# Kernel tuning notes

Hardware: AMD Instinct MI355X
Metric: run time of the kernel (lower is better)

The kernel has to match this reference:

```python
import jax, jax.numpy as jnp
import numpy as np

N_NODES = 100000
IN_F = 128
H_F = 128
LOOKBACK = 3
N_EDGES = 640000


def setup_inputs() -> dict:
    key = jax.random.key(0)
    ks = jax.random.split(key, 16)
    s = lambda k, shp: jax.random.normal(k, shp, dtype=jnp.float32) * 0.05
    inp = {
        "feat": jax.random.normal(ks[0], (N_NODES, IN_F), dtype=jnp.float32),
        "edges": jax.random.randint(ks[1], (LOOKBACK, 2, N_EDGES), 0, N_NODES, dtype=jnp.int32),
        # conv1 (SAGEConv pool, in->h) params
        "Wp1": s(ks[2], (IN_F, IN_F)), "bp1": jnp.zeros((IN_F,), jnp.float32),
        "Ws1": s(ks[3], (H_F, IN_F)), "Wn1": s(ks[4], (H_F, IN_F)), "b1": jnp.zeros((H_F,), jnp.float32),
        # BatchNorm1d affine params (training-mode batch stats)
        "gamma": jnp.ones((H_F,), jnp.float32), "beta": jnp.zeros((H_F,), jnp.float32),
        # conv2 (SAGEConv pool, h->h) params
        "Wp2": s(ks[5], (H_F, H_F)), "bp2": jnp.zeros((H_F,), jnp.float32),
        "Ws2": s(ks[6], (H_F, H_F)), "Wn2": s(ks[7], (H_F, H_F)), "b2": jnp.zeros((H_F,), jnp.float32),
    }
    return inp


def _sage_pool_conv(h, src, dst, Wp, bp, Ws, Wn, b):
    # pool aggregator: m = relu(fc_pool(h)); neigh = max over in-edges
    m = jax.nn.relu(h @ Wp.T + bp)                      # [N, d]
    agg = jax.ops.segment_max(m[src], dst, num_segments=N_NODES)  # [N, d]
    agg = jnp.where(jnp.isfinite(agg), agg, 0.0)        # nodes with no in-edges -> 0
    return h @ Ws.T + agg @ Wn.T + b


def _batchnorm(x, gamma, beta, eps=1e-5):
    mu = jnp.mean(x, axis=0)
    var = jnp.var(x, axis=0)
    return (x - mu) * jax.lax.rsqrt(var + eps) * gamma + beta


def reference(feat, edges, Wp1, bp1, Ws1, Wn1, b1, gamma, beta, Wp2, bp2, Ws2, Wn2, b2):
    def per_graph(e):
        src, dst = e[0], e[1]
        h = _sage_pool_conv(feat, src, dst, Wp1, bp1, Ws1, Wn1, b1)
        h = _batchnorm(h, gamma, beta)
        h = jax.nn.relu(h)
        h = _sage_pool_conv(h, src, dst, Wp2, bp2, Ws2, Wn2, b2)
        return h

    return jax.vmap(per_graph)(edges)  # [lookback, N, H_F]
```

## Files before the change

### kernel.cpp

```cpp
#include <hip/hip_runtime.h>
#include <hip/hip_bf16.h>

#define NNODES 100000
#define FD 128
#define NEDGES 640000
#define NB 391
#define GEMM_GRID 782
#define OFFS_U32 100032

typedef __bf16 bf16x8 __attribute__((ext_vector_type(8)));
typedef __bf16 bf16x4 __attribute__((ext_vector_type(4)));
typedef float f32x4 __attribute__((ext_vector_type(4)));
typedef unsigned short u16x8 __attribute__((ext_vector_type(8)));

__device__ __forceinline__ bf16x8 cvt8(float4 a, float4 b) {
  bf16x8 r;
  r[0] = (__bf16)a.x; r[1] = (__bf16)a.y; r[2] = (__bf16)a.z; r[3] = (__bf16)a.w;
  r[4] = (__bf16)b.x; r[5] = (__bf16)b.y; r[6] = (__bf16)b.z; r[7] = (__bf16)b.w;
  return r;
}

__global__ __launch_bounds__(256) void packw6_k(
    const float* __restrict__ W0, const float* __restrict__ W1,
    const float* __restrict__ W2, const float* __restrict__ W3,
    const float* __restrict__ W4, const float* __restrict__ W5,
    __bf16* __restrict__ out) {
  const int gidx = blockIdx.x * 256 + threadIdx.x;
  const int wi = gidx >> 11;
  const int f = gidx & 2047;
  const float* W = wi == 0 ? W0 : wi == 1 ? W1 : wi == 2 ? W2
                 : wi == 3 ? W3 : wi == 4 ? W4 : W5;
  const int c = f >> 8, kk = (f >> 6) & 3, lane = f & 63;
  const int lr = lane & 15, lg = lane >> 4;
  const float* p = W + (c * 16 + lr) * FD + kk * 32 + lg * 8;
  *(bf16x8*)(out + (long)gidx * 8) = cvt8(*(const float4*)p, *(const float4*)(p + 4));
}

template <int AM>
__device__ __forceinline__ void load_arow(const void* __restrict__ A, long row,
                                          int kbase, const float* __restrict__ scsh,
                                          bf16x8 (&af)[4]) {
  if constexpr (AM == 1) {
#pragma unroll
    for (int kk = 0; kk < 4; ++kk)
      af[kk] = *(const bf16x8*)((const __bf16*)A + row * FD + kbase + kk * 32);
  } else if constexpr (AM == 3) {
#pragma unroll
    for (int kk = 0; kk < 4; ++kk) {
      const int k = kbase + kk * 32;
      const bf16x8 r = *(const bf16x8*)((const __bf16*)A + row * FD + k);
      const float4 scx = *(const float4*)(scsh + k);
      const float4 scy = *(const float4*)(scsh + k + 4);
      const float4 shx = *(const float4*)(scsh + 128 + k);
      const float4 shy = *(const float4*)(scsh + 128 + k + 4);
      bf16x8 o;
      o[0] = (__bf16)fmaxf((float)r[0] * scx.x + shx.x, 0.f);
      o[1] = (__bf16)fmaxf((float)r[1] * scx.y + shx.y, 0.f);
      o[2] = (__bf16)fmaxf((float)r[2] * scx.z + shx.z, 0.f);
      o[3] = (__bf16)fmaxf((float)r[3] * scx.w + shx.w, 0.f);
      o[4] = (__bf16)fmaxf((float)r[4] * scy.x + shy.x, 0.f);
      o[5] = (__bf16)fmaxf((float)r[5] * scy.y + shy.y, 0.f);
      o[6] = (__bf16)fmaxf((float)r[6] * scy.z + shy.z, 0.f);
      o[7] = (__bf16)fmaxf((float)r[7] * scy.w + shy.w, 0.f);
      af[kk] = o;
    }
  } else {
#pragma unroll
    for (int kk = 0; kk < 4; ++kk) {
      const int k = kbase + kk * 32;
      const float* ap = (const float*)A + row * FD + k;
      af[kk] = cvt8(*(const float4*)ap, *(const float4*)(ap + 4));
    }
  }
}

template <int A0M, int A1M, bool TWOA, bool RELU, bool OUTBF16, bool STATS, bool WRITEB>
__global__ __launch_bounds__(256, 3) void gemm_k(
    const void* __restrict__ A0, long a0s, const void* __restrict__ A1, long a1s,
    const __bf16* __restrict__ W0p, const __bf16* __restrict__ W1p,
    const float* __restrict__ bias, const float* __restrict__ scsh0,
    void* __restrict__ outp, long os, float* __restrict__ pblk,
    __bf16* __restrict__ bcopy, int M) {
  const int g = blockIdx.y;
  const int wid = threadIdx.x >> 6;
  const int lane = threadIdx.x & 63;
  const int lr = lane & 15;
  const int lg = lane >> 4;
  const int kbase = lg * 8;
  const int rbase = blockIdx.x * 128 + wid * 32;
  __shared__ float s_red[2][4][128];

  const void* A0g = (const char*)A0 + (long)g * a0s;
  const void* A1g = (const char*)A1 + (TWOA ? (long)g * a1s : 0);
  void* outg = (char*)outp + (long)g * os;
  const float* scshg = (A0M == 3 || A1M == 3) ? scsh0 + (long)g * 256 : nullptr;
  float* pblkg = STATS ? pblk + (long)g * ((long)GEMM_GRID * 256) : nullptr;

  if constexpr (!STATS) {
    if (rbase >= M) return;
  }

  f32x4 acc[2][8];
#pragma unroll
  for (int t = 0; t < 2; ++t)
#pragma unroll
    for (int c = 0; c < 8; ++c) acc[t][c] = (f32x4){0.f, 0.f, 0.f, 0.f};

  {
    bf16x8 a0[2][4];
#pragma unroll
    for (int t = 0; t < 2; ++t) {
      long row = rbase + t * 16 + lr;
      if (row > M - 1) row = M - 1;
      load_arow<A0M>(A0g, row, kbase, scshg, a0[t]);
    }
    if constexpr (WRITEB) {
#pragma unroll
      for (int t = 0; t < 2; ++t) {
        const int row = rbase + t * 16 + lr;
        if (row < M)
#pragma unroll
          for (int kk = 0; kk < 4; ++kk)
            *(bf16x8*)(bcopy + (long)row * FD + kbase + kk * 32) = a0[t][kk];
      }
    }
#pragma unroll
    for (int c = 0; c < 8; ++c) {
      bf16x8 bw[4];
#pragma unroll
      for (int kk = 0; kk < 4; ++kk)
        bw[kk] = *(const bf16x8*)(W0p + ((long)((c * 4 + kk) * 64 + lane)) * 8);
#pragma unroll
      for (int t = 0; t < 2; ++t)
#pragma unroll
        for (int kk = 0; kk < 4; ++kk)
          acc[t][c] = __builtin_amdgcn_mfma_f32_16x16x32_bf16(bw[kk], a0[t][kk], acc[t][c], 0, 0, 0);
    }
  }
  if constexpr (TWOA) {
    bf16x8 a1[2][4];
#pragma unroll
    for (int t = 0; t < 2; ++t) {
      long row = rbase + t * 16 + lr;
      if (row > M - 1) row = M - 1;
      load_arow<A1M>(A1g, row, kbase, scshg, a1[t]);
    }
#pragma unroll
    for (int c = 0; c < 8; ++c) {
      bf16x8 bw[4];
#pragma unroll
      for (int kk = 0; kk < 4; ++kk)
        bw[kk] = *(const bf16x8*)(W1p + ((long)((c * 4 + kk) * 64 + lane)) * 8);
#pragma unroll
      for (int t = 0; t < 2; ++t)
#pragma unroll
        for (int kk = 0; kk < 4; ++kk)
          acc[t][c] = __builtin_amdgcn_mfma_f32_16x16x32_bf16(bw[kk], a1[t][kk], acc[t][c], 0, 0, 0);
    }
  }

  float ps[8][4], pss[8][4];
  if constexpr (STATS) {
#pragma unroll
    for (int c = 0; c < 8; ++c)
#pragma unroll
      for (int j = 0; j < 4; ++j) { ps[c][j] = 0.f; pss[c][j] = 0.f; }
  }

#pragma unroll
  for (int t = 0; t < 2; ++t) {
    const int row = rbase + t * 16 + lr;
    const bool ok = row < M;
#pragma unroll
    for (int c = 0; c < 8; ++c) {
      const int cb = c * 16 + lg * 4;
      f32x4 v = acc[t][c];
      if (bias) {
        const float4 bv = *(const float4*)(bias + cb);
        v[0] += bv.x; v[1] += bv.y; v[2] += bv.z; v[3] += bv.w;
      }
      if constexpr (STATS) {
        if (ok) {
#pragma unroll
          for (int j = 0; j < 4; ++j) { ps[c][j] += v[j]; pss[c][j] += v[j] * v[j]; }
        }
      }
      if constexpr (RELU) {
#pragma unroll
        for (int j = 0; j < 4; ++j) v[j] = fmaxf(v[j], 0.f);
      }
      if (ok) {
        if constexpr (OUTBF16) {
          bf16x4 o;
          o[0] = (__bf16)v[0]; o[1] = (__bf16)v[1];
          o[2] = (__bf16)v[2]; o[3] = (__bf16)v[3];
          *(bf16x4*)((__bf16*)outg + (long)row * FD + cb) = o;
        } else {
          *(f32x4*)((float*)outg + (long)row * FD + cb) = v;
        }
      }
    }
  }

  if constexpr (STATS) {
#pragma unroll
    for (int c = 0; c < 8; ++c)
#pragma unroll
      for (int j = 0; j < 4; ++j) {
        float s = ps[c][j], q = pss[c][j];
        s += __shfl_xor(s, 1); s += __shfl_xor(s, 2);
        s += __shfl_xor(s, 4); s += __shfl_xor(s, 8);
        q += __shfl_xor(q, 1); q += __shfl_xor(q, 2);
        q += __shfl_xor(q, 4); q += __shfl_xor(q, 8);
        if (lr == 0) {
          s_red[0][wid][c * 16 + lg * 4 + j] = s;
          s_red[1][wid][c * 16 + lg * 4 + j] = q;
        }
      }
    __syncthreads();
    const int tid = threadIdx.x;
    const int which = tid >> 7, col = tid & 127;
    pblkg[(long)blockIdx.x * 256 + tid] =
        s_red[which][0][col] + s_red[which][1][col] + s_red[which][2][col] + s_red[which][3][col];
  }
}

__global__ __launch_bounds__(256) void bn_red1_k(const float* __restrict__ pblk,
                                                 float* __restrict__ pblk2) {
  const int g = blockIdx.y;
  const float* p = pblk + (long)g * GEMM_GRID * 256;
  float s = 0.f;
  for (int r = blockIdx.x; r < GEMM_GRID; r += 64) s += p[(long)r * 256 + threadIdx.x];
  pblk2[((long)g * 64 + blockIdx.x) * 256 + threadIdx.x] = s;
}

__global__ __launch_bounds__(256) void bn_final2_k(const float* __restrict__ pblk2,
                                                   const float* __restrict__ gamma,
                                                   const float* __restrict__ beta,
                                                   float* __restrict__ scsh3) {
  __shared__ float s_ss[128];
  const int g = blockIdx.y;
  const int tid = threadIdx.x;
  const float* p = pblk2 + (long)g * 64 * 256;
  float s = 0.f;
#pragma unroll
  for (int r = 0; r < 64; ++r) s += p[r * 256 + tid];
  if (tid >= 128) s_ss[tid - 128] = s;
  __syncthreads();
  if (tid < 128) {
    const float mu = s / (float)NNODES;
    const float var = s_ss[tid] / (float)NNODES - mu * mu;
    const float sc = rsqrtf(var + 1e-5f) * gamma[tid];
    scsh3[g * 256 + tid] = sc;
    scsh3[g * 256 + 128 + tid] = beta[tid] - mu * sc;
  }
}


__global__ __launch_bounds__(256) void hist_rank3_k(const int* __restrict__ edges,
                                                    unsigned* __restrict__ deg3,
                                                    unsigned short* __restrict__ rank3) {
  const int g = blockIdx.y;
  const int e = blockIdx.x * 256 + threadIdx.x;
  if (e < NEDGES) {
    const int d = edges[(long)g * 2 * NEDGES + NEDGES + e];
    const unsigned r = atomicAdd(&deg3[(long)g * NNODES + d], 1u);
    rank3[(long)g * NEDGES + e] = (unsigned short)r;
  }
}

__global__ __launch_bounds__(256) void blocksum3_k(const unsigned* __restrict__ deg3,
                                                   unsigned* __restrict__ bsum3) {
  __shared__ unsigned s[256];
  const int g = blockIdx.y;
  const int i = blockIdx.x * 256 + threadIdx.x;
  s[threadIdx.x] = (i < NNODES) ? deg3[(long)g * NNODES + i] : 0u;
  __syncthreads();
#pragma unroll
  for (int o = 128; o > 0; o >>= 1) {
    if (threadIdx.x < o) s[threadIdx.x] += s[threadIdx.x + o];
    __syncthreads();
  }
  if (threadIdx.x == 0) bsum3[g * NB + blockIdx.x] = s[0];
}

__global__ __launch_bounds__(512) void scanb3_k(const unsigned* __restrict__ bsum3,
                                                unsigned* __restrict__ boffs3,
                                                unsigned* __restrict__ offs3) {
  __shared__ unsigned s[512];
  const int g = blockIdx.y;
  const unsigned v = (threadIdx.x < NB) ? bsum3[g * NB + threadIdx.x] : 0u;
  s[threadIdx.x] = v;
  __syncthreads();
#pragma unroll
  for (int o = 1; o < 512; o <<= 1) {
    unsigned t = (threadIdx.x >= o) ? s[threadIdx.x - o] : 0u;
    __syncthreads();
    s[threadIdx.x] += t;
    __syncthreads();
  }
  if (threadIdx.x < NB) boffs3[g * NB + threadIdx.x] = s[threadIdx.x] - v;
  if (threadIdx.x == 0) offs3[(long)g * OFFS_U32 + NNODES] = NEDGES;
}

__global__ __launch_bounds__(256) void offsets3_k(const unsigned* __restrict__ deg3,
                                                  const unsigned* __restrict__ boffs3,
                                                  unsigned* __restrict__ offs3) {
  __shared__ unsigned s[256];
  const int g = blockIdx.y;
  const int i = blockIdx.x * 256 + threadIdx.x;
  const unsigned v = (i < NNODES) ? deg3[(long)g * NNODES + i] : 0u;
  s[threadIdx.x] = v;
  __syncthreads();
#pragma unroll
  for (int o = 1; o < 256; o <<= 1) {
    unsigned t = (threadIdx.x >= o) ? s[threadIdx.x - o] : 0u;
    __syncthreads();
    s[threadIdx.x] += t;
    __syncthreads();
  }
  const unsigned excl = s[threadIdx.x] - v + boffs3[g * NB + blockIdx.x];
  if (i < NNODES) offs3[(long)g * OFFS_U32 + i] = excl;
}

__global__ __launch_bounds__(256) void scat3_k(const int* __restrict__ edges,
                                               const unsigned* __restrict__ offs3,
                                               const unsigned short* __restrict__ rank3,
                                               int* __restrict__ ssrc3) {
  const int g = blockIdx.y;
  const int e = blockIdx.x * 256 + threadIdx.x;
  if (e < NEDGES) {
    const int s = edges[(long)g * 2 * NEDGES + e];
    const int d = edges[(long)g * 2 * NEDGES + NEDGES + e];
    const unsigned p = offs3[(long)g * OFFS_U32 + d] + rank3[(long)g * NEDGES + e];
    ssrc3[(long)g * NEDGES + p] = s;
  }
}

__global__ __launch_bounds__(256) void agg_k(const unsigned short* __restrict__ m,
                                             long ms, const int* __restrict__ ssrc3,
                                             const unsigned* __restrict__ offs3,
                                             unsigned short* __restrict__ agg3) {
  const int g = blockIdx.y;
  const unsigned short* mg = m + (long)g * ms;
  const int* ssrc = ssrc3 + (long)g * NEDGES;
  const unsigned* offs = offs3 + (long)g * OFFS_U32;
  unsigned short* agg = agg3 + (long)g * NNODES * FD;

  const int gid = blockIdx.x * 256 + threadIdx.x;
  const int node = gid >> 4;
  if (node >= NNODES) return;
  const int fl = (gid & 15) * 8;
  const unsigned beg = offs[node], end = offs[node + 1];
  u16x8 acc = {0, 0, 0, 0, 0, 0, 0, 0};
  unsigned i = beg;
  for (; i + 2 <= end; i += 2) {
    const int s0 = ssrc[i];
    const int s1 = ssrc[i + 1];
    const u16x8 v0 = *(const u16x8*)(mg + (long)s0 * FD + fl);
    const u16x8 v1 = *(const u16x8*)(mg + (long)s1 * FD + fl);
#pragma unroll
    for (int j = 0; j < 8; ++j) {
      const unsigned short mx = v0[j] > v1[j] ? v0[j] : v1[j];
      acc[j] = mx > acc[j] ? mx : acc[j];
    }
  }
  if (i < end) {
    const u16x8 v = *(const u16x8*)(mg + (long)ssrc[i] * FD + fl);
#pragma unroll
    for (int j = 0; j < 8; ++j) acc[j] = v[j] > acc[j] ? v[j] : acc[j];
  }
  *(u16x8*)(agg + (long)node * FD + fl) = acc;
}

__global__ __launch_bounds__(256) void zero_k(float4* __restrict__ p, long n4) {
  const long i = (long)blockIdx.x * 256 + threadIdx.x;
  if (i < n4) p[i] = (float4){0.f, 0.f, 0.f, 0.f};
}

extern "C" void kernel_launch(void* const* d_in, const int* in_sizes, int n_in,
                              void* d_out, int out_size, void* d_ws, size_t ws_size,
                              hipStream_t stream) {
  const float* feat = (const float*)d_in[0];
  const int* edges = (const int*)d_in[1];
  const float* Wp1 = (const float*)d_in[2];
  const float* bp1 = (const float*)d_in[3];
  const float* Ws1 = (const float*)d_in[4];
  const float* Wn1 = (const float*)d_in[5];
  const float* b1 = (const float*)d_in[6];
  const float* gamma = (const float*)d_in[7];
  const float* beta = (const float*)d_in[8];
  const float* Wp2 = (const float*)d_in[9];
  const float* bp2 = (const float*)d_in[10];
  const float* Ws2 = (const float*)d_in[11];
  const float* Wn2 = (const float*)d_in[12];
  const float* b2 = (const float*)d_in[13];

  const long SZ_BF = 25600000;
  const long SZ_F32 = 51200000;

  char* w = (char*)d_ws;
  __bf16* m1 = (__bf16*)w;
  __bf16* featb = (__bf16*)(w + 25600000);
  __bf16* h1b3 = (__bf16*)(w + 51200000);
  __bf16* aggb3 = (__bf16*)(w + 128000000);
  __bf16* m2_3 = (__bf16*)(w + 204800000);
  __bf16* wpk = (__bf16*)(w + 281600000);
  unsigned* deg3 = (unsigned*)(w + 281796608);
  unsigned* offs3 = (unsigned*)(w + 282996608);
  unsigned* bsum3 = (unsigned*)(w + 284196992);
  unsigned* boffs3 = (unsigned*)(w + 284201728);
  unsigned short* rank3 = (unsigned short*)(w + 284206464);
  int* ssrc3 = (int*)(w + 288046464);
  float* pblk3 = (float*)(w + 295726464);
  float* pblk2_3 = (float*)(w + 298128768);
  float* scsh3 = (float*)(w + 298325376);

  __bf16* Wp1p = wpk;
  __bf16* Ws1p = wpk + 16384;
  __bf16* Wn1p = wpk + 2 * 16384;
  __bf16* Wp2p = wpk + 3 * 16384;
  __bf16* Ws2p = wpk + 4 * 16384;
  __bf16* Wn2p = wpk + 5 * 16384;

  const dim3 blk(256);
  const int edgeGrid = (NEDGES + 255) / 256;
  const int aggGrid = (NNODES * 16 + 255) / 256;
  const int degZeroGrid = (3 * NNODES / 4 + 255) / 256;

  packw6_k<<<48, blk, 0, stream>>>(Wp1, Ws1, Wn1, Wp2, Ws2, Wn2, wpk);

  zero_k<<<degZeroGrid, blk, 0, stream>>>((float4*)deg3, 3L * NNODES / 4);
  hist_rank3_k<<<dim3(edgeGrid, 3), blk, 0, stream>>>(edges, deg3, rank3);
  blocksum3_k<<<dim3(NB, 3), blk, 0, stream>>>(deg3, bsum3);
  scanb3_k<<<dim3(1, 3), dim3(512), 0, stream>>>(bsum3, boffs3, offs3);
  offsets3_k<<<dim3(NB, 3), blk, 0, stream>>>(deg3, boffs3, offs3);
  scat3_k<<<dim3(edgeGrid, 3), blk, 0, stream>>>(edges, offs3, rank3, ssrc3);

  gemm_k<0, 0, false, true, true, false, true><<<dim3(GEMM_GRID, 1), blk, 0, stream>>>(
      feat, 0, nullptr, 0, Wp1p, nullptr, bp1, nullptr, m1, 0, nullptr, featb, NNODES);

  agg_k<<<dim3(aggGrid, 3), blk, 0, stream>>>((const unsigned short*)m1, 0L,
                                              ssrc3, offs3, (unsigned short*)aggb3);
  gemm_k<1, 1, true, false, true, true, false><<<dim3(GEMM_GRID, 3), blk, 0, stream>>>(
      aggb3, SZ_BF, featb, 0, Wn1p, Ws1p, b1, nullptr, h1b3, SZ_BF, pblk3, nullptr, NNODES);
  bn_red1_k<<<dim3(64, 3), blk, 0, stream>>>(pblk3, pblk2_3);
  bn_final2_k<<<dim3(1, 3), blk, 0, stream>>>(pblk2_3, gamma, beta, scsh3);

  gemm_k<3, 0, false, true, true, false, false><<<dim3(GEMM_GRID, 3), blk, 0, stream>>>(
      h1b3, SZ_BF, nullptr, 0, Wp2p, nullptr, bp2, scsh3, m2_3, SZ_BF, nullptr, nullptr, NNODES);
  agg_k<<<dim3(aggGrid, 3), blk, 0, stream>>>((const unsigned short*)m2_3,
                                              (long)NNODES * FD, ssrc3, offs3,
                                              (unsigned short*)aggb3);
  gemm_k<3, 1, true, false, false, false, false><<<dim3(GEMM_GRID, 3), blk, 0, stream>>>(
      h1b3, SZ_BF, aggb3, SZ_BF, Ws2p, Wn2p, b2, scsh3, d_out, SZ_F32, nullptr, nullptr, NNODES);
}
```

Measured before the change: 582.8 us.

## Make GEMMs persistent with LDS-cached weights, double-buffered loads, separate BN stats pass

Rewrites the GEMM kernel as a persistent grid-stride loop. Each block stages the packed bf16 weights in LDS once and double-buffers A-row chunk loads so the next chunk's global loads overlap the current MFMA work. The fused BatchNorm statistic accumulation is taken out of the GEMM and replaced by a standalone stats kernel that rereads the bf16 h1 output. The final fp32 output uses nontemporal stores. This trades an extra read of h1 and lower occupancy (launch bounds 2, larger LDS) for less weight traffic and better latency hiding.

```diff
diff --git a/kernel.cpp b/kernel.cpp
--- a/kernel.cpp
+++ b/kernel.cpp
@@ -5,8 +5,10 @@
 #define FD 128
 #define NEDGES 640000
 #define NB 391
-#define GEMM_GRID 782
+#define CPG 782
+#define GX 172
 #define OFFS_U32 100032
+#define BNST 128
 
 typedef __bf16 bf16x8 __attribute__((ext_vector_type(8)));
 typedef __bf16 bf16x4 __attribute__((ext_vector_type(4)));
@@ -74,164 +76,178 @@
   }
 }
 
-template <int A0M, int A1M, bool TWOA, bool RELU, bool OUTBF16, bool STATS, bool WRITEB>
-__global__ __launch_bounds__(256, 3) void gemm_k(
-    const void* __restrict__ A0, long a0s, const void* __restrict__ A1, long a1s,
-    const __bf16* __restrict__ W0p, const __bf16* __restrict__ W1p,
-    const float* __restrict__ bias, const float* __restrict__ scsh0,
-    void* __restrict__ outp, long os, float* __restrict__ pblk,
-    __bf16* __restrict__ bcopy, int M) {
-  const int g = blockIdx.y;
-  const int wid = threadIdx.x >> 6;
-  const int lane = threadIdx.x & 63;
-  const int lr = lane & 15;
-  const int lg = lane >> 4;
-  const int kbase = lg * 8;
-  const int rbase = blockIdx.x * 128 + wid * 32;
-  __shared__ float s_red[2][4][128];
-
-  const void* A0g = (const char*)A0 + (long)g * a0s;
-  const void* A1g = (const char*)A1 + (TWOA ? (long)g * a1s : 0);
-  void* outg = (char*)outp + (long)g * os;
-  const float* scshg = (A0M == 3 || A1M == 3) ? scsh0 + (long)g * 256 : nullptr;
-  float* pblkg = STATS ? pblk + (long)g * ((long)GEMM_GRID * 256) : nullptr;
-
-  if constexpr (!STATS) {
-    if (rbase >= M) return;
-  }
-
-  f32x4 acc[2][8];
-#pragma unroll
-  for (int t = 0; t < 2; ++t)
-#pragma unroll
-    for (int c = 0; c < 8; ++c) acc[t][c] = (f32x4){0.f, 0.f, 0.f, 0.f};
-
-  {
-    bf16x8 a0[2][4];
-#pragma unroll
-    for (int t = 0; t < 2; ++t) {
-      long row = rbase + t * 16 + lr;
-      if (row > M - 1) row = M - 1;
-      load_arow<A0M>(A0g, row, kbase, scshg, a0[t]);
-    }
-    if constexpr (WRITEB) {
-#pragma unroll
-      for (int t = 0; t < 2; ++t) {
-        const int row = rbase + t * 16 + lr;
-        if (row < M)
-#pragma unroll
-          for (int kk = 0; kk < 4; ++kk)
-            *(bf16x8*)(bcopy + (long)row * FD + kbase + kk * 32) = a0[t][kk];
-      }
-    }
-#pragma unroll
-    for (int c = 0; c < 8; ++c) {
-      bf16x8 bw[4];
+template <int AM>
+__device__ __forceinline__ void load_chunk(const void* __restrict__ A, int ch,
+                                           int wid, int lr, int kbase,
+                                           const float* __restrict__ scsh,
+                                           bf16x8 (&af)[2][4], int M) {
+  const int rbase = ch * 128 + wid * 32;
+#pragma unroll
+  for (int t = 0; t < 2; ++t) {
+    long row = rbase + t * 16 + lr;
+    if (row > M - 1) row = M - 1;
+    load_arow<AM>(A, row, kbase, scsh, af[t]);
+  }
+}
+
+__device__ __forceinline__ void mma_pass_lds(const __bf16* __restrict__ wl, int lane,
+                                             const bf16x8 (&af)[2][4],
+                                             f32x4 (&acc)[2][8]) {
+#pragma unroll
+  for (int c = 0; c < 8; ++c) {
+    bf16x8 bw[4];
+#pragma unroll
+    for (int kk = 0; kk < 4; ++kk)
+      bw[kk] = *(const bf16x8*)(wl + ((long)((c * 4 + kk) * 64 + lane)) * 8);
+#pragma unroll
+    for (int t = 0; t < 2; ++t)
 #pragma unroll
       for (int kk = 0; kk < 4; ++kk)
-        bw[kk] = *(const bf16x8*)(W0p + ((long)((c * 4 + kk) * 64 + lane)) * 8);
-#pragma unroll
-      for (int t = 0; t < 2; ++t)
-#pragma unroll
-        for (int kk = 0; kk < 4; ++kk)
-          acc[t][c] = __builtin_amdgcn_mfma_f32_16x16x32_bf16(bw[kk], a0[t][kk], acc[t][c], 0, 0, 0);
-    }
-  }
-  if constexpr (TWOA) {
-    bf16x8 a1[2][4];
-#pragma unroll
-    for (int t = 0; t < 2; ++t) {
-      long row = rbase + t * 16 + lr;
-      if (row > M - 1) row = M - 1;
-      load_arow<A1M>(A1g, row, kbase, scshg, a1[t]);
-    }
-#pragma unroll
-    for (int c = 0; c < 8; ++c) {
-      bf16x8 bw[4];
-#pragma unroll
-      for (int kk = 0; kk < 4; ++kk)
-        bw[kk] = *(const bf16x8*)(W1p + ((long)((c * 4 + kk) * 64 + lane)) * 8);
-#pragma unroll
-      for (int t = 0; t < 2; ++t)
-#pragma unroll
-        for (int kk = 0; kk < 4; ++kk)
-          acc[t][c] = __builtin_amdgcn_mfma_f32_16x16x32_bf16(bw[kk], a1[t][kk], acc[t][c], 0, 0, 0);
-    }
-  }
-
-  float ps[8][4], pss[8][4];
-  if constexpr (STATS) {
-#pragma unroll
-    for (int c = 0; c < 8; ++c)
-#pragma unroll
-      for (int j = 0; j < 4; ++j) { ps[c][j] = 0.f; pss[c][j] = 0.f; }
-  }
-
+        acc[t][c] = __builtin_amdgcn_mfma_f32_16x16x32_bf16(bw[kk], af[t][kk], acc[t][c], 0, 0, 0);
+  }
+}
+
+template <bool RELU, bool OUTBF16, bool NT>
+__device__ __forceinline__ void epilogue(f32x4 (&acc)[2][8], int ch, int wid,
+                                         int lr, int lg,
+                                         const float* __restrict__ bias,
+                                         void* __restrict__ outg, int M) {
+  const int rbase = ch * 128 + wid * 32;
 #pragma unroll
   for (int t = 0; t < 2; ++t) {
     const int row = rbase + t * 16 + lr;
-    const bool ok = row < M;
-#pragma unroll
-    for (int c = 0; c < 8; ++c) {
-      const int cb = c * 16 + lg * 4;
-      f32x4 v = acc[t][c];
-      if (bias) {
+    if (row < M) {
+#pragma unroll
+      for (int c = 0; c < 8; ++c) {
+        const int cb = c * 16 + lg * 4;
+        f32x4 v = acc[t][c];
         const float4 bv = *(const float4*)(bias + cb);
         v[0] += bv.x; v[1] += bv.y; v[2] += bv.z; v[3] += bv.w;
-      }
-      if constexpr (STATS) {
-        if (ok) {
-#pragma unroll
-          for (int j = 0; j < 4; ++j) { ps[c][j] += v[j]; pss[c][j] += v[j] * v[j]; }
+        if constexpr (RELU) {
+#pragma unroll
+          for (int j = 0; j < 4; ++j) v[j] = fmaxf(v[j], 0.f);
         }
-      }
-      if constexpr (RELU) {
-#pragma unroll
-        for (int j = 0; j < 4; ++j) v[j] = fmaxf(v[j], 0.f);
-      }
-      if (ok) {
         if constexpr (OUTBF16) {
           bf16x4 o;
           o[0] = (__bf16)v[0]; o[1] = (__bf16)v[1];
           o[2] = (__bf16)v[2]; o[3] = (__bf16)v[3];
           *(bf16x4*)((__bf16*)outg + (long)row * FD + cb) = o;
         } else {
-          *(f32x4*)((float*)outg + (long)row * FD + cb) = v;
+          f32x4* p = (f32x4*)((float*)outg + (long)row * FD + cb);
+          if constexpr (NT) __builtin_nontemporal_store(v, p);
+          else *p = v;
         }
       }
     }
   }
-
-  if constexpr (STATS) {
-#pragma unroll
-    for (int c = 0; c < 8; ++c)
-#pragma unroll
-      for (int j = 0; j < 4; ++j) {
-        float s = ps[c][j], q = pss[c][j];
-        s += __shfl_xor(s, 1); s += __shfl_xor(s, 2);
-        s += __shfl_xor(s, 4); s += __shfl_xor(s, 8);
-        q += __shfl_xor(q, 1); q += __shfl_xor(q, 2);
-        q += __shfl_xor(q, 4); q += __shfl_xor(q, 8);
-        if (lr == 0) {
-          s_red[0][wid][c * 16 + lg * 4 + j] = s;
-          s_red[1][wid][c * 16 + lg * 4 + j] = q;
-        }
-      }
-    __syncthreads();
-    const int tid = threadIdx.x;
-    const int which = tid >> 7, col = tid & 127;
-    pblkg[(long)blockIdx.x * 256 + tid] =
-        s_red[which][0][col] + s_red[which][1][col] + s_red[which][2][col] + s_red[which][3][col];
-  }
-}
-
-__global__ __launch_bounds__(256) void bn_red1_k(const float* __restrict__ pblk,
-                                                 float* __restrict__ pblk2) {
-  const int g = blockIdx.y;
-  const float* p = pblk + (long)g * GEMM_GRID * 256;
-  float s = 0.f;
-  for (int r = blockIdx.x; r < GEMM_GRID; r += 64) s += p[(long)r * 256 + threadIdx.x];
-  pblk2[((long)g * 64 + blockIdx.x) * 256 + threadIdx.x] = s;
+}
+
+__device__ __forceinline__ void write_bcopy(const bf16x8 (&af)[2][4], int ch,
+                                            int wid, int lr, int kbase,
+                                            __bf16* __restrict__ bcopy, int M) {
+  const int rbase = ch * 128 + wid * 32;
+#pragma unroll
+  for (int t = 0; t < 2; ++t) {
+    const int row = rbase + t * 16 + lr;
+    if (row < M) {
+#pragma unroll
+      for (int kk = 0; kk < 4; ++kk)
+        *(bf16x8*)(bcopy + (long)row * FD + kbase + kk * 32) = af[t][kk];
+    }
+  }
+}
+
+template <int A0M, int A1M, bool TWOA, bool RELU, bool OUTBF16, bool WRITEB, bool NT>
+__global__ __launch_bounds__(256, 2) void gemm_k(
+    const void* __restrict__ A0, long a0s, const void* __restrict__ A1, long a1s,
+    const __bf16* __restrict__ W0p, const __bf16* __restrict__ W1p,
+    const float* __restrict__ bias, const float* __restrict__ scsh0,
+    void* __restrict__ outp, long os, __bf16* __restrict__ bcopy, int M) {
+  __shared__ __align__(16) __bf16 wlds[(TWOA ? 2 : 1) * 16384];
+  const int g = blockIdx.y;
+  const int wid = threadIdx.x >> 6;
+  const int lane = threadIdx.x & 63;
+  const int lr = lane & 15;
+  const int lg = lane >> 4;
+  const int kbase = lg * 8;
+  const int S = gridDim.x;
+
+  const void* A0g = (const char*)A0 + (long)g * a0s;
+  const void* A1g = TWOA ? ((const char*)A1 + (long)g * a1s) : nullptr;
+  void* outg = (char*)outp + (long)g * os;
+  const float* scshg = (A0M == 3 || A1M == 3) ? (scsh0 + (long)g * 256) : nullptr;
+
+  bf16x8 a0A[2][4], a0B[2][4];
+  bf16x8 a1A[2][4], a1B[2][4];
+
+  const int ch0 = blockIdx.x;
+  load_chunk<A0M>(A0g, ch0, wid, lr, kbase, scshg, a0A, M);
+  if constexpr (TWOA) load_chunk<A1M>(A1g, ch0, wid, lr, kbase, scshg, a1A, M);
+
+  for (int it = threadIdx.x; it < 2048; it += 256)
+    *(bf16x8*)(wlds + (long)it * 8) = *(const bf16x8*)(W0p + (long)it * 8);
+  if constexpr (TWOA) {
+    for (int it = threadIdx.x; it < 2048; it += 256)
+      *(bf16x8*)(wlds + 16384 + (long)it * 8) = *(const bf16x8*)(W1p + (long)it * 8);
+  }
+  __syncthreads();
+
+  f32x4 acc[2][8];
+  for (int ch = ch0; ch < CPG; ch += 2 * S) {
+    const int chB = ch + S;
+    load_chunk<A0M>(A0g, chB, wid, lr, kbase, scshg, a0B, M);
+    if constexpr (TWOA) load_chunk<A1M>(A1g, chB, wid, lr, kbase, scshg, a1B, M);
+#pragma unroll
+    for (int t = 0; t < 2; ++t)
+#pragma unroll
+      for (int c = 0; c < 8; ++c) acc[t][c] = (f32x4){0.f, 0.f, 0.f, 0.f};
+    mma_pass_lds(wlds, lane, a0A, acc);
+    if constexpr (TWOA) mma_pass_lds(wlds + 16384, lane, a1A, acc);
+    if constexpr (WRITEB) write_bcopy(a0A, ch, wid, lr, kbase, bcopy, M);
+    epilogue<RELU, OUTBF16, NT>(acc, ch, wid, lr, lg, bias, outg, M);
+    load_chunk<A0M>(A0g, ch + 2 * S, wid, lr, kbase, scshg, a0A, M);
+    if constexpr (TWOA) load_chunk<A1M>(A1g, ch + 2 * S, wid, lr, kbase, scshg, a1A, M);
+#pragma unroll
+    for (int t = 0; t < 2; ++t)
+#pragma unroll
+      for (int c = 0; c < 8; ++c) acc[t][c] = (f32x4){0.f, 0.f, 0.f, 0.f};
+    mma_pass_lds(wlds, lane, a0B, acc);
+    if constexpr (TWOA) mma_pass_lds(wlds + 16384, lane, a1B, acc);
+    if constexpr (WRITEB) write_bcopy(a0B, chB, wid, lr, kbase, bcopy, M);
+    epilogue<RELU, OUTBF16, NT>(acc, chB, wid, lr, lg, bias, outg, M);
+  }
+}
+
+__global__ __launch_bounds__(256) void bn_stats1_k(const __bf16* __restrict__ h3,
+                                                   float* __restrict__ pblk2) {
+  const int g = blockIdx.y;
+  const __bf16* h = h3 + (long)g * NNODES * FD;
+  const int tid = threadIdx.x;
+  const int cb = (tid & 15) * 8;
+  const int rg = tid >> 4;
+  float s[8], ss[8];
+#pragma unroll
+  for (int j = 0; j < 8; ++j) { s[j] = 0.f; ss[j] = 0.f; }
+  for (int r = blockIdx.x * 16 + rg; r < NNODES; r += BNST * 16) {
+    const bf16x8 v = *(const bf16x8*)(h + (long)r * FD + cb);
+#pragma unroll
+    for (int j = 0; j < 8; ++j) {
+      const float x = (float)v[j];
+      s[j] += x;
+      ss[j] += x * x;
+    }
+  }
+  __shared__ float ls[16][256];
+#pragma unroll
+  for (int j = 0; j < 8; ++j) {
+    ls[rg][cb + j] = s[j];
+    ls[rg][128 + cb + j] = ss[j];
+  }
+  __syncthreads();
+  float a = 0.f;
+#pragma unroll
+  for (int q = 0; q < 16; ++q) a += ls[q][tid];
+  pblk2[((long)g * BNST + blockIdx.x) * 256 + tid] = a;
 }
 
 __global__ __launch_bounds__(256) void bn_final2_k(const float* __restrict__ pblk2,
@@ -241,10 +257,9 @@
   __shared__ float s_ss[128];
   const int g = blockIdx.y;
   const int tid = threadIdx.x;
-  const float* p = pblk2 + (long)g * 64 * 256;
+  const float* p = pblk2 + (long)g * BNST * 256;
   float s = 0.f;
-#pragma unroll
-  for (int r = 0; r < 64; ++r) s += p[r * 256 + tid];
+  for (int r = 0; r < BNST; ++r) s += p[r * 256 + tid];
   if (tid >= 128) s_ss[tid - 128] = s;
   __syncthreads();
   if (tid < 128) {
@@ -412,9 +427,8 @@
   unsigned* boffs3 = (unsigned*)(w + 284201728);
   unsigned short* rank3 = (unsigned short*)(w + 284206464);
   int* ssrc3 = (int*)(w + 288046464);
-  float* pblk3 = (float*)(w + 295726464);
-  float* pblk2_3 = (float*)(w + 298128768);
-  float* scsh3 = (float*)(w + 298325376);
+  float* pblk2 = (float*)(w + 295726464);
+  float* scsh3 = (float*)(w + 296126464);
 
   __bf16* Wp1p = wpk;
   __bf16* Ws1p = wpk + 16384;
@@ -437,21 +451,22 @@
   offsets3_k<<<dim3(NB, 3), blk, 0, stream>>>(deg3, boffs3, offs3);
   scat3_k<<<dim3(edgeGrid, 3), blk, 0, stream>>>(edges, offs3, rank3, ssrc3);
 
-  gemm_k<0, 0, false, true, true, false, true><<<dim3(GEMM_GRID, 1), blk, 0, stream>>>(
-      feat, 0, nullptr, 0, Wp1p, nullptr, bp1, nullptr, m1, 0, nullptr, featb, NNODES);
+  gemm_k<0, 0, false, true, true, true, false><<<dim3(391, 1), blk, 0, stream>>>(
+      feat, 0, nullptr, 0, Wp1p, nullptr, bp1, nullptr, m1, 0, featb, NNODES);
 
   agg_k<<<dim3(aggGrid, 3), blk, 0, stream>>>((const unsigned short*)m1, 0L,
                                               ssrc3, offs3, (unsigned short*)aggb3);
-  gemm_k<1, 1, true, false, true, true, false><<<dim3(GEMM_GRID, 3), blk, 0, stream>>>(
-      aggb3, SZ_BF, featb, 0, Wn1p, Ws1p, b1, nullptr, h1b3, SZ_BF, pblk3, nullptr, NNODES);
-  bn_red1_k<<<dim3(64, 3), blk, 0, stream>>>(pblk3, pblk2_3);
-  bn_final2_k<<<dim3(1, 3), blk, 0, stream>>>(pblk2_3, gamma, beta, scsh3);
-
-  gemm_k<3, 0, false, true, true, false, false><<<dim3(GEMM_GRID, 3), blk, 0, stream>>>(
-      h1b3, SZ_BF, nullptr, 0, Wp2p, nullptr, bp2, scsh3, m2_3, SZ_BF, nullptr, nullptr, NNODES);
+  gemm_k<1, 1, true, false, true, false, false><<<dim3(GX, 3), blk, 0, stream>>>(
+      aggb3, SZ_BF, featb, 0, Wn1p, Ws1p, b1, nullptr, h1b3, SZ_BF, nullptr, NNODES);
+
+  bn_stats1_k<<<dim3(BNST, 3), blk, 0, stream>>>(h1b3, pblk2);
+  bn_final2_k<<<dim3(1, 3), blk, 0, stream>>>(pblk2, gamma, beta, scsh3);
+
+  gemm_k<3, 0, false, true, true, false, false><<<dim3(GX, 3), blk, 0, stream>>>(
+      h1b3, SZ_BF, nullptr, 0, Wp2p, nullptr, bp2, scsh3, m2_3, SZ_BF, nullptr, NNODES);
   agg_k<<<dim3(aggGrid, 3), blk, 0, stream>>>((const unsigned short*)m2_3,
                                               (long)NNODES * FD, ssrc3, offs3,
                                               (unsigned short*)aggb3);
-  gemm_k<3, 1, true, false, false, false, false><<<dim3(GEMM_GRID, 3), blk, 0, stream>>>(
-      h1b3, SZ_BF, aggb3, SZ_BF, Ws2p, Wn2p, b2, scsh3, d_out, SZ_F32, nullptr, nullptr, NNODES);
-}
+  gemm_k<3, 1, true, false, false, false, true><<<dim3(GX, 3), blk, 0, stream>>>(
+      h1b3, SZ_BF, aggb3, SZ_BF, Ws2p, Wn2p, b2, scsh3, d_out, SZ_F32, nullptr, NNODES);
+}
```

Result: slower. 1.036 ms (+77.7%).

## Split GEMM output columns across waves, halve rows per block, raise occupancy

Applied to the files above, without the earlier changes.

Each GEMM block now covers 64 rows instead of 128, and its four waves form a 2x2 grid where each wave computes half of the 128 output columns. This halves the accumulator registers per wave, so launch bounds rise from 3 to 4 blocks per SM, and the grid doubles to expose more parallelism. The cost is that every A row is loaded by two waves, so A-tile global reads double. The BN partial-stat buffers are moved into the m2 region to fit the larger grid's partials.

```diff
diff --git a/kernel.cpp b/kernel.cpp
--- a/kernel.cpp
+++ b/kernel.cpp
@@ -5,8 +5,9 @@
 #define FD 128
 #define NEDGES 640000
 #define NB 391
-#define GEMM_GRID 782
+#define GRID1 1564
 #define OFFS_U32 100032
+#define BNRED 64
 
 typedef __bf16 bf16x8 __attribute__((ext_vector_type(8)));
 typedef __bf16 bf16x4 __attribute__((ext_vector_type(4)));
@@ -75,7 +76,7 @@
 }
 
 template <int A0M, int A1M, bool TWOA, bool RELU, bool OUTBF16, bool STATS, bool WRITEB>
-__global__ __launch_bounds__(256, 3) void gemm_k(
+__global__ __launch_bounds__(256, 4) void gemm_k(
     const void* __restrict__ A0, long a0s, const void* __restrict__ A1, long a1s,
     const __bf16* __restrict__ W0p, const __bf16* __restrict__ W1p,
     const float* __restrict__ bias, const float* __restrict__ scsh0,
@@ -83,28 +84,30 @@
     __bf16* __restrict__ bcopy, int M) {
   const int g = blockIdx.y;
   const int wid = threadIdx.x >> 6;
+  const int rw = wid & 1;
+  const int cw = wid >> 1;
   const int lane = threadIdx.x & 63;
   const int lr = lane & 15;
   const int lg = lane >> 4;
   const int kbase = lg * 8;
-  const int rbase = blockIdx.x * 128 + wid * 32;
-  __shared__ float s_red[2][4][128];
+  const int rbase = blockIdx.x * 64 + rw * 32;
+  __shared__ float s_red[2][4][64];
 
   const void* A0g = (const char*)A0 + (long)g * a0s;
   const void* A1g = (const char*)A1 + (TWOA ? (long)g * a1s : 0);
   void* outg = (char*)outp + (long)g * os;
   const float* scshg = (A0M == 3 || A1M == 3) ? scsh0 + (long)g * 256 : nullptr;
-  float* pblkg = STATS ? pblk + (long)g * ((long)GEMM_GRID * 256) : nullptr;
+  float* pblkg = STATS ? pblk + (long)g * ((long)GRID1 * 256) : nullptr;
 
   if constexpr (!STATS) {
     if (rbase >= M) return;
   }
 
-  f32x4 acc[2][8];
+  f32x4 acc[2][4];
 #pragma unroll
   for (int t = 0; t < 2; ++t)
 #pragma unroll
-    for (int c = 0; c < 8; ++c) acc[t][c] = (f32x4){0.f, 0.f, 0.f, 0.f};
+    for (int c = 0; c < 4; ++c) acc[t][c] = (f32x4){0.f, 0.f, 0.f, 0.f};
 
   {
     bf16x8 a0[2][4];
@@ -115,21 +118,23 @@
       load_arow<A0M>(A0g, row, kbase, scshg, a0[t]);
     }
     if constexpr (WRITEB) {
-#pragma unroll
-      for (int t = 0; t < 2; ++t) {
-        const int row = rbase + t * 16 + lr;
-        if (row < M)
-#pragma unroll
-          for (int kk = 0; kk < 4; ++kk)
-            *(bf16x8*)(bcopy + (long)row * FD + kbase + kk * 32) = a0[t][kk];
-      }
-    }
-#pragma unroll
-    for (int c = 0; c < 8; ++c) {
+      if (cw == 0) {
+#pragma unroll
+        for (int t = 0; t < 2; ++t) {
+          const int row = rbase + t * 16 + lr;
+          if (row < M)
+#pragma unroll
+            for (int kk = 0; kk < 4; ++kk)
+              *(bf16x8*)(bcopy + (long)row * FD + kbase + kk * 32) = a0[t][kk];
+        }
+      }
+    }
+#pragma unroll
+    for (int c = 0; c < 4; ++c) {
       bf16x8 bw[4];
 #pragma unroll
       for (int kk = 0; kk < 4; ++kk)
-        bw[kk] = *(const bf16x8*)(W0p + ((long)((c * 4 + kk) * 64 + lane)) * 8);
+        bw[kk] = *(const bf16x8*)(W0p + ((long)(((cw * 4 + c) * 4 + kk) * 64 + lane)) * 8);
 #pragma unroll
       for (int t = 0; t < 2; ++t)
 #pragma unroll
@@ -146,11 +151,11 @@
       load_arow<A1M>(A1g, row, kbase, scshg, a1[t]);
     }
 #pragma unroll
-    for (int c = 0; c < 8; ++c) {
+    for (int c = 0; c < 4; ++c) {
       bf16x8 bw[4];
 #pragma unroll
       for (int kk = 0; kk < 4; ++kk)
-        bw[kk] = *(const bf16x8*)(W1p + ((long)((c * 4 + kk) * 64 + lane)) * 8);
+        bw[kk] = *(const bf16x8*)(W1p + ((long)(((cw * 4 + c) * 4 + kk) * 64 + lane)) * 8);
 #pragma unroll
       for (int t = 0; t < 2; ++t)
 #pragma unroll
@@ -159,10 +164,10 @@
     }
   }
 
-  float ps[8][4], pss[8][4];
+  float ps[4][4], pss[4][4];
   if constexpr (STATS) {
 #pragma unroll
-    for (int c = 0; c < 8; ++c)
+    for (int c = 0; c < 4; ++c)
 #pragma unroll
       for (int j = 0; j < 4; ++j) { ps[c][j] = 0.f; pss[c][j] = 0.f; }
   }
@@ -172,8 +177,8 @@
     const int row = rbase + t * 16 + lr;
     const bool ok = row < M;
 #pragma unroll
-    for (int c = 0; c < 8; ++c) {
-      const int cb = c * 16 + lg * 4;
+    for (int c = 0; c < 4; ++c) {
+      const int cb = cw * 64 + c * 16 + lg * 4;
       f32x4 v = acc[t][c];
       if (bias) {
         const float4 bv = *(const float4*)(bias + cb);
@@ -204,7 +209,7 @@
 
   if constexpr (STATS) {
 #pragma unroll
-    for (int c = 0; c < 8; ++c)
+    for (int c = 0; c < 4; ++c)
 #pragma unroll
       for (int j = 0; j < 4; ++j) {
         float s = ps[c][j], q = pss[c][j];
@@ -219,19 +224,20 @@
       }
     __syncthreads();
     const int tid = threadIdx.x;
-    const int which = tid >> 7, col = tid & 127;
+    const int wh = tid >> 7, cg = tid & 127;
+    const int cwi = cg >> 6, cl = cg & 63;
     pblkg[(long)blockIdx.x * 256 + tid] =
-        s_red[which][0][col] + s_red[which][1][col] + s_red[which][2][col] + s_red[which][3][col];
+        s_red[wh][cwi * 2 + 0][cl] + s_red[wh][cwi * 2 + 1][cl];
   }
 }
 
 __global__ __launch_bounds__(256) void bn_red1_k(const float* __restrict__ pblk,
                                                  float* __restrict__ pblk2) {
   const int g = blockIdx.y;
-  const float* p = pblk + (long)g * GEMM_GRID * 256;
+  const float* p = pblk + (long)g * GRID1 * 256;
   float s = 0.f;
-  for (int r = blockIdx.x; r < GEMM_GRID; r += 64) s += p[(long)r * 256 + threadIdx.x];
-  pblk2[((long)g * 64 + blockIdx.x) * 256 + threadIdx.x] = s;
+  for (int r = blockIdx.x; r < GRID1; r += BNRED) s += p[(long)r * 256 + threadIdx.x];
+  pblk2[((long)g * BNRED + blockIdx.x) * 256 + threadIdx.x] = s;
 }
 
 __global__ __launch_bounds__(256) void bn_final2_k(const float* __restrict__ pblk2,
@@ -241,10 +247,10 @@
   __shared__ float s_ss[128];
   const int g = blockIdx.y;
   const int tid = threadIdx.x;
-  const float* p = pblk2 + (long)g * 64 * 256;
+  const float* p = pblk2 + (long)g * BNRED * 256;
   float s = 0.f;
 #pragma unroll
-  for (int r = 0; r < 64; ++r) s += p[r * 256 + tid];
+  for (int r = 0; r < BNRED; ++r) s += p[r * 256 + tid];
   if (tid >= 128) s_ss[tid - 128] = s;
   __syncthreads();
   if (tid < 128) {
@@ -405,16 +411,16 @@
   __bf16* h1b3 = (__bf16*)(w + 51200000);
   __bf16* aggb3 = (__bf16*)(w + 128000000);
   __bf16* m2_3 = (__bf16*)(w + 204800000);
+  float* pblk3 = (float*)(w + 204800000);
+  float* pblk2_3 = (float*)(w + 209604608);
   __bf16* wpk = (__bf16*)(w + 281600000);
-  unsigned* deg3 = (unsigned*)(w + 281796608);
-  unsigned* offs3 = (unsigned*)(w + 282996608);
-  unsigned* bsum3 = (unsigned*)(w + 284196992);
-  unsigned* boffs3 = (unsigned*)(w + 284201728);
-  unsigned short* rank3 = (unsigned short*)(w + 284206464);
-  int* ssrc3 = (int*)(w + 288046464);
-  float* pblk3 = (float*)(w + 295726464);
-  float* pblk2_3 = (float*)(w + 298128768);
-  float* scsh3 = (float*)(w + 298325376);
+  float* scsh3 = (float*)(w + 281796608);
+  unsigned* deg3 = (unsigned*)(w + 281799680);
+  unsigned* offs3 = (unsigned*)(w + 282999680);
+  unsigned* bsum3 = (unsigned*)(w + 284200064);
+  unsigned* boffs3 = (unsigned*)(w + 284204928);
+  unsigned short* rank3 = (unsigned short*)(w + 284209792);
+  int* ssrc3 = (int*)(w + 288049792);
 
   __bf16* Wp1p = wpk;
   __bf16* Ws1p = wpk + 16384;
@@ -437,21 +443,21 @@
   offsets3_k<<<dim3(NB, 3), blk, 0, stream>>>(deg3, boffs3, offs3);
   scat3_k<<<dim3(edgeGrid, 3), blk, 0, stream>>>(edges, offs3, rank3, ssrc3);
 
-  gemm_k<0, 0, false, true, true, false, true><<<dim3(GEMM_GRID, 1), blk, 0, stream>>>(
+  gemm_k<0, 0, false, true, true, false, true><<<dim3(GRID1, 1), blk, 0, stream>>>(
       feat, 0, nullptr, 0, Wp1p, nullptr, bp1, nullptr, m1, 0, nullptr, featb, NNODES);
 
   agg_k<<<dim3(aggGrid, 3), blk, 0, stream>>>((const unsigned short*)m1, 0L,
                                               ssrc3, offs3, (unsigned short*)aggb3);
-  gemm_k<1, 1, true, false, true, true, false><<<dim3(GEMM_GRID, 3), blk, 0, stream>>>(
+  gemm_k<1, 1, true, false, true, true, false><<<dim3(GRID1, 3), blk, 0, stream>>>(
       aggb3, SZ_BF, featb, 0, Wn1p, Ws1p, b1, nullptr, h1b3, SZ_BF, pblk3, nullptr, NNODES);
-  bn_red1_k<<<dim3(64, 3), blk, 0, stream>>>(pblk3, pblk2_3);
+  bn_red1_k<<<dim3(BNRED, 3), blk, 0, stream>>>(pblk3, pblk2_3);
   bn_final2_k<<<dim3(1, 3), blk, 0, stream>>>(pblk2_3, gamma, beta, scsh3);
 
-  gemm_k<3, 0, false, true, true, false, false><<<dim3(GEMM_GRID, 3), blk, 0, stream>>>(
+  gemm_k<3, 0, false, true, true, false, false><<<dim3(GRID1, 3), blk, 0, stream>>>(
       h1b3, SZ_BF, nullptr, 0, Wp2p, nullptr, bp2, scsh3, m2_3, SZ_BF, nullptr, nullptr, NNODES);
   agg_k<<<dim3(aggGrid, 3), blk, 0, stream>>>((const unsigned short*)m2_3,
                                               (long)NNODES * FD, ssrc3, offs3,
                                               (unsigned short*)aggb3);
-  gemm_k<3, 1, true, false, false, false, false><<<dim3(GEMM_GRID, 3), blk, 0, stream>>>(
+  gemm_k<3, 1, true, false, false, false, false><<<dim3(GRID1, 3), blk, 0, stream>>>(
       h1b3, SZ_BF, aggb3, SZ_BF, Ws2p, Wn2p, b2, scsh3, d_out, SZ_F32, nullptr, nullptr, NNODES);
 }
```

After: 569.2 us. -2.3%, faster.
